# Optimization experiments

Hardware: AMD Instinct MI355X
Metric: run time of the kernel (lower is better)

Reference implementation:

```python
import jax, jax.numpy as jnp
import numpy as np

S = 10        # spiking_segment_count
TEMP = 50.0

def setup_inputs() -> dict:
    key = jax.random.key(0)
    ks = jax.random.split(key, 6)
    bs, din, dout = 2048, 1024, 1024
    x = jax.random.normal(ks[0], (bs, din), dtype=jnp.float32)
    t = jax.random.uniform(ks[1], (bs,), dtype=jnp.float32)  # in [0,1) subset of [-1,1]
    scale = 1.0 / np.sqrt(din)
    param_W = jax.random.normal(ks[2], (din, dout * S * 3), dtype=jnp.float32) * scale
    param_b = jax.random.normal(ks[3], (dout * S * 3,), dtype=jnp.float32) * 0.01
    norm_W = jax.random.normal(ks[4], (din, dout), dtype=jnp.float32) * scale
    norm_b = jax.random.normal(ks[5], (dout,), dtype=jnp.float32) * 0.01
    return {"x": x, "t": t, "param_W": param_W, "param_b": param_b,
            "norm_W": norm_W, "norm_b": norm_b}

def reference(x, t, param_W, param_b, norm_W, norm_b):
    bs = x.shape[0]
    dout = norm_W.shape[1]
    # param GEMM -> (bs, S, dout, 3)
    params = (x @ param_W + param_b).reshape(bs, S, dout, 3)
    weights = jax.nn.softmax(params[..., 0], axis=1)                 # (bs, S, dout)
    keypoints = jnp.concatenate(
        [jnp.zeros_like(weights[:, :1]), jnp.cumsum(weights, axis=1)], axis=1
    ) * 2.0 - 1.0                                                    # (bs, S+1, dout)
    slopes = jnp.tanh(params[..., 1])
    intercepts = params[..., 2]
    tt = t.reshape(-1, 1, 1)                                         # (bs, 1, 1)
    starts = keypoints[:, :S]
    ends = keypoints[:, 1:]
    residual = slopes * tt + intercepts                              # (bs, S, dout)
    validity = ((tt >= starts) & (tt < ends)) | ((tt == 1.0) & (ends == 1.0))
    vf = validity.astype(x.dtype)
    left_margin = jnp.sum((tt - starts) * vf, axis=1)                # (bs, dout)
    right_margin = jnp.sum((ends - tt) * vf, axis=1)
    lw = jax.nn.sigmoid(-TEMP * left_margin)
    rw = jax.nn.sigmoid(-TEMP * right_margin)
    lv = jnp.concatenate([vf[:, :1], vf[:, :-1]], axis=1)
    rv = jnp.concatenate([vf[:, 1:], vf[:, -1:]], axis=1)
    sw = -(lw + rw - 1.0)
    result = (lw * jnp.sum(residual * lv, axis=1)
              + sw * jnp.sum(residual * vf, axis=1)
              + rw * jnp.sum(residual * rv, axis=1))
    # norm == 'constant': subtract segment-wise integral, add norm_net(x)
    integral = jnp.sum(0.5 * slopes * (ends * ends - starts * starts)
                       + intercepts * weights, axis=1) * 0.5
    norm_target = x @ norm_W + norm_b
    return result - integral + norm_target
```

## Files before the change

### kernel.cpp

```cpp
#include <hip/hip_runtime.h>
#include <cstdint>
#include <cstddef>

#define BS    2048
#define DIN   1024
#define DOUT  1024
#define SSEG  10
#define NPAR  30720
#define NPK   20480
#define NCOL2 21504
#define NLG   10240
#define TAU   5e-5f
#define WL_CAP 1048576u

typedef _Float16 half_t;
typedef __attribute__((ext_vector_type(8))) _Float16 half8;
typedef __attribute__((ext_vector_type(4))) _Float16 half4;
typedef __attribute__((ext_vector_type(4))) float   floatx4;

__device__ __forceinline__ void gload16(const void* g, void* l) {
  __builtin_amdgcn_global_load_lds(
      (const __attribute__((address_space(1))) void*)g,
      (__attribute__((address_space(3))) void*)l, 16, 0, 0);
}

__global__ void k_zero(unsigned* c) { if (threadIdx.x == 0) *c = 0; }

__global__ __launch_bounds__(256) void k_split_x(const float* __restrict__ x,
                                                 half_t* __restrict__ xh,
                                                 half_t* __restrict__ xl) {
  int i = blockIdx.x * 256 + threadIdx.x;
  floatx4 v = ((const floatx4*)x)[i];
  half4 h, l;
  #pragma unroll
  for (int c = 0; c < 4; c++) { h[c] = (half_t)v[c]; l[c] = (half_t)(v[c] - (float)h[c]); }
  ((half4*)xh)[i] = h;
  ((half4*)xl)[i] = l;
}

__global__ __launch_bounds__(256) void k_transpose_pk(const float* __restrict__ src,
                                                      half_t* __restrict__ dst) {
  __shared__ float tile[32][33];
  int tx = threadIdx.x & 31;
  int ty = threadIdx.x >> 5;
  int c0 = blockIdx.x * 32;
  int k0 = blockIdx.y * 32;
  int j = c0 + tx;
  int s = j >> 11, rem = j & 2047;
  int scol = s * 3072 + 3 * (rem >> 1) + 1 + (rem & 1);
  #pragma unroll
  for (int r = ty; r < 32; r += 8)
    tile[r][tx] = src[(size_t)(k0 + r) * NPAR + scol];
  __syncthreads();
  #pragma unroll
  for (int r = ty; r < 32; r += 8)
    dst[(size_t)(c0 + r) * DIN + k0 + tx] = (half_t)tile[tx][r];
}

__global__ __launch_bounds__(256) void k_transpose(const float* __restrict__ src,
                                                   half_t* __restrict__ dst,
                                                   int ncols, int col_off) {
  __shared__ float tile[32][33];
  int tx = threadIdx.x & 31;
  int ty = threadIdx.x >> 5;
  int col0 = blockIdx.x * 32;
  int k0   = blockIdx.y * 32;
  #pragma unroll
  for (int r = ty; r < 32; r += 8)
    tile[r][tx] = src[(size_t)(k0 + r) * ncols + col0 + tx];
  __syncthreads();
  #pragma unroll
  for (int r = ty; r < 32; r += 8)
    dst[(size_t)(col0 + r + col_off) * DIN + k0 + tx] = (half_t)tile[tx][r];
}

__global__ __launch_bounds__(256) void k_transpose_logit(const float* __restrict__ src,
                                                         half_t* __restrict__ dh,
                                                         half_t* __restrict__ dl,
                                                         float* __restrict__ wlt) {
  __shared__ float tile[32][33];
  int tx = threadIdx.x & 31;
  int ty = threadIdx.x >> 5;
  int c0 = blockIdx.x * 32;
  int k0 = blockIdx.y * 32;
  int lcol = c0 + tx;
  int scol = (lcol >> 10) * 3072 + (lcol & 1023) * 3;
  #pragma unroll
  for (int r = ty; r < 32; r += 8)
    tile[r][tx] = src[(size_t)(k0 + r) * NPAR + scol];
  __syncthreads();
  #pragma unroll
  for (int r = ty; r < 32; r += 8) {
    float raw = tile[tx][r];
    float v = raw * 32.0f;
    half_t h = (half_t)v;
    half_t l = (half_t)(v - (float)h);
    dh [(size_t)(c0 + r) * DIN + k0 + tx] = h;
    dl [(size_t)(c0 + r) * DIN + k0 + tx] = l;
    wlt[(size_t)(c0 + r) * DIN + k0 + tx] = raw;
  }
}

__global__ __launch_bounds__(256) void k_gemm(const half_t* __restrict__ A,
                                              const half_t* __restrict__ B,
                                              float* __restrict__ C,
                                              const float* __restrict__ pb,
                                              const float* __restrict__ nb) {
  __shared__ __attribute__((aligned(16))) half_t As[128 * 32];
  __shared__ __attribute__((aligned(16))) half_t Bs[128 * 32];
  const int K = DIN;
  int m0 = blockIdx.y * 128, n0 = blockIdx.x * 128;
  int tid = threadIdx.x, w = tid >> 6, L = tid & 63;
  int wm = (w >> 1) * 64, wn = (w & 1) * 64;
  int l15 = L & 15, quad = L >> 4;

  const half_t* ga = A + (size_t)(m0 + w * 16 + (L >> 2)) * K + (L & 3) * 8;
  const half_t* gb = B + (size_t)(n0 + w * 16 + (L >> 2)) * K + (L & 3) * 8;
  char* lA = (char*)As + w * 1024;
  char* lB = (char*)Bs + w * 1024;

  floatx4 acc[4][4] = {};

  for (int k0 = 0; k0 < K; k0 += 32) {
    __syncthreads();
    gload16(ga + k0,          lA);
    gload16(ga + 64 * K + k0, lA + 4096);
    gload16(gb + k0,          lB);
    gload16(gb + 64 * K + k0, lB + 4096);
    __syncthreads();

    half8 af[4], bf[4];
    #pragma unroll
    for (int mi = 0; mi < 4; mi++)
      af[mi] = *(const half8*)((const char*)As + (wm + mi * 16 + l15) * 64 + quad * 16);
    #pragma unroll
    for (int ni = 0; ni < 4; ni++)
      bf[ni] = *(const half8*)((const char*)Bs + (wn + ni * 16 + l15) * 64 + quad * 16);
    #pragma unroll
    for (int mi = 0; mi < 4; mi++)
      #pragma unroll
      for (int ni = 0; ni < 4; ni++)
        acc[mi][ni] = __builtin_amdgcn_mfma_f32_16x16x32_f16(af[mi], bf[ni], acc[mi][ni], 0, 0, 0);
  }

  #pragma unroll
  for (int ni = 0; ni < 4; ni++) {
    int col = n0 + wn + ni * 16 + l15;
    float bias;
    if (col < NPK) {
      int s = col >> 11, rem = col & 2047;
      bias = pb[s * 3072 + 3 * (rem >> 1) + 1 + (rem & 1)];
    } else {
      bias = nb[col - NPK];
    }
    #pragma unroll
    for (int mi = 0; mi < 4; mi++) {
      int row = m0 + wm + mi * 16 + quad * 4;
      floatx4 v = acc[mi][ni];
      #pragma unroll
      for (int r = 0; r < 4; r++)
        C[(size_t)(row + r) * NCOL2 + col] = v[r] + bias;
    }
  }
}

__global__ __launch_bounds__(256) void k_gemm_logit(const half_t* __restrict__ Ah,
                                                    const half_t* __restrict__ Al,
                                                    const half_t* __restrict__ Bh,
                                                    const half_t* __restrict__ Bl,
                                                    float* __restrict__ Lg,
                                                    const float* __restrict__ pb) {
  __shared__ __attribute__((aligned(16))) half_t sAh[128 * 32];
  __shared__ __attribute__((aligned(16))) half_t sAl[128 * 32];
  __shared__ __attribute__((aligned(16))) half_t sBh[128 * 32];
  __shared__ __attribute__((aligned(16))) half_t sBl[128 * 32];
  const int K = DIN;
  int m0 = blockIdx.y * 128, n0 = blockIdx.x * 128;
  int tid = threadIdx.x, w = tid >> 6, L = tid & 63;
  int wm = (w >> 1) * 64, wn = (w & 1) * 64;
  int l15 = L & 15, quad = L >> 4;

  size_t aoff = (size_t)(m0 + w * 16 + (L >> 2)) * K + (L & 3) * 8;
  size_t boff = (size_t)(n0 + w * 16 + (L >> 2)) * K + (L & 3) * 8;
  char* lah = (char*)sAh + w * 1024;
  char* lal = (char*)sAl + w * 1024;
  char* lbh = (char*)sBh + w * 1024;
  char* lbl = (char*)sBl + w * 1024;

  floatx4 acc[4][4] = {};

  for (int k0 = 0; k0 < K; k0 += 32) {
    __syncthreads();
    gload16(Ah + aoff + k0,          lah);
    gload16(Ah + aoff + 64 * K + k0, lah + 4096);
    gload16(Al + aoff + k0,          lal);
    gload16(Al + aoff + 64 * K + k0, lal + 4096);
    gload16(Bh + boff + k0,          lbh);
    gload16(Bh + boff + 64 * K + k0, lbh + 4096);
    gload16(Bl + boff + k0,          lbl);
    gload16(Bl + boff + 64 * K + k0, lbl + 4096);
    __syncthreads();

    #pragma unroll
    for (int mi = 0; mi < 4; mi++) {
      half8 afh = *(const half8*)((const char*)sAh + (wm + mi * 16 + l15) * 64 + quad * 16);
      half8 afl = *(const half8*)((const char*)sAl + (wm + mi * 16 + l15) * 64 + quad * 16);
      #pragma unroll
      for (int ni = 0; ni < 4; ni++) {
        half8 bfh = *(const half8*)((const char*)sBh + (wn + ni * 16 + l15) * 64 + quad * 16);
        half8 bfl = *(const half8*)((const char*)sBl + (wn + ni * 16 + l15) * 64 + quad * 16);
        floatx4 a = acc[mi][ni];
        a = __builtin_amdgcn_mfma_f32_16x16x32_f16(afh, bfh, a, 0, 0, 0);
        a = __builtin_amdgcn_mfma_f32_16x16x32_f16(afl, bfh, a, 0, 0, 0);
        a = __builtin_amdgcn_mfma_f32_16x16x32_f16(afh, bfl, a, 0, 0, 0);
        acc[mi][ni] = a;
      }
    }
  }

  #pragma unroll
  for (int ni = 0; ni < 4; ni++) {
    int col = n0 + wn + ni * 16 + l15;
    float bias = pb[(col >> 10) * 3072 + (col & 1023) * 3];
    #pragma unroll
    for (int mi = 0; mi < 4; mi++) {
      int row = m0 + wm + mi * 16 + quad * 4;
      floatx4 v = acc[mi][ni];
      #pragma unroll
      for (int r = 0; r < 4; r++)
        Lg[(size_t)(row + r) * NLG + col] = v[r] * 0.03125f + bias;
    }
  }
}

__device__ __forceinline__ float spiking_eval(const float* p, float tt, float* mind) {
  float mx = -1e30f;
  #pragma unroll
  for (int s = 0; s < SSEG; s++) mx = fmaxf(mx, p[3 * s]);
  float ew[10], wsum = 0.0f;
  #pragma unroll
  for (int s = 0; s < SSEG; s++) { ew[s] = __expf(p[3 * s] - mx); wsum += ew[s]; }
  float inv = 1.0f / wsum;

  float kp[11];
  kp[0] = -1.0f;
  float cum = 0.0f, md = 1e30f;
  #pragma unroll
  for (int s = 0; s < SSEG; s++) {
    cum += ew[s] * inv;
    kp[s + 1] = cum * 2.0f - 1.0f;
    md = fminf(md, fabsf(tt - kp[s + 1]));
  }
  *mind = md;

  float vf[10], resid[10];
  float lm = 0.0f, rm = 0.0f, integ = 0.0f;
  #pragma unroll
  for (int s = 0; s < SSEG; s++) {
    float p1 = p[3 * s + 1], p2 = p[3 * s + 2];
    float e2 = __expf(2.0f * fabsf(p1));
    float th = copysignf(1.0f - 2.0f / (e2 + 1.0f), p1);
    resid[s] = th * tt + p2;
    float st = kp[s], en = kp[s + 1];
    bool v = ((tt >= st) && (tt < en)) || ((tt == 1.0f) && (en == 1.0f));
    float vv = v ? 1.0f : 0.0f;
    vf[s] = vv;
    lm += (tt - st) * vv;
    rm += (en - tt) * vv;
    integ += 0.5f * th * (en * en - st * st) + p2 * (ew[s] * inv);
  }
  float resLV = 0.0f, resV = 0.0f, resRV = 0.0f;
  #pragma unroll
  for (int s = 0; s < SSEG; s++) {
    float lv = (s == 0) ? vf[0] : vf[s - 1];
    float rv = (s == 9) ? vf[9] : vf[s + 1];
    resLV += resid[s] * lv;
    resV  += resid[s] * vf[s];
    resRV += resid[s] * rv;
  }
  float lw = 1.0f / (1.0f + __expf(50.0f * lm));
  float rw = 1.0f / (1.0f + __expf(50.0f * rm));
  float swt = 1.0f - lw - rw;
  return lw * resLV + swt * resV + rw * resRV - 0.5f * integ + p[30];
}

__global__ __launch_bounds__(256) void k_pointwise(const float* __restrict__ P,
                                                   const float* __restrict__ Lg,
                                                   const float* __restrict__ t,
                                                   float* __restrict__ out,
                                                   unsigned* __restrict__ cnt,
                                                   unsigned* __restrict__ wl,
                                                   unsigned cap) {
  __shared__ __attribute__((aligned(16))) float sp[SSEG * 512];
  int b = blockIdx.x, dg = blockIdx.y, tid = threadIdx.x;
  const float* Pb = P + (size_t)b * NCOL2;
  for (int i = tid; i < SSEG * 128; i += 256) {
    int s = i >> 7, e = i & 127;
    ((floatx4*)sp)[s * 128 + e] = ((const floatx4*)(Pb + s * 2048 + dg * 512))[e];
  }
  float tt = t[b];
  float nt = Pb[NPK + dg * 256 + tid];
  const float* Lb = Lg + (size_t)b * NLG + dg * 256 + tid;
  __syncthreads();

  float p[31];
  #pragma unroll
  for (int s = 0; s < SSEG; s++) {
    p[3 * s]     = Lb[s * 1024];
    p[3 * s + 1] = sp[s * 512 + 2 * tid];
    p[3 * s + 2] = sp[s * 512 + 2 * tid + 1];
  }
  p[30] = nt;
  float mind;
  float r = spiking_eval(p, tt, &mind);
  int d = dg * 256 + tid;
  out[(size_t)b * DOUT + d] = r;
  if (wl != nullptr && mind < TAU) {
    unsigned idx = atomicAdd(cnt, 1u);
    if (idx < cap) wl[idx] = ((unsigned)b << 10) | (unsigned)d;
  }
}

__global__ __launch_bounds__(256) void k_naive(const float* __restrict__ x,
                                               const float* __restrict__ t,
                                               const float* __restrict__ pW,
                                               const float* __restrict__ pb,
                                               const float* __restrict__ nW,
                                               const float* __restrict__ nb,
                                               float* __restrict__ out,
                                               unsigned* __restrict__ cnt,
                                               unsigned* __restrict__ wl,
                                               unsigned cap) {
  __shared__ float xs[DIN];
  int b = blockIdx.x, dg = blockIdx.y, tid = threadIdx.x;
  for (int i = tid; i < DIN; i += 256) xs[i] = x[(size_t)b * DIN + i];
  __syncthreads();
  int d = dg * 256 + tid;
  float acc[31];
  #pragma unroll
  for (int i = 0; i < 31; i++) acc[i] = 0.0f;
  for (int k = 0; k < DIN; k++) {
    float xv = xs[k];
    const float* wr = pW + (size_t)k * NPAR + 3 * d;
    #pragma unroll
    for (int s = 0; s < SSEG; s++) {
      acc[3 * s]     += xv * wr[s * 3072];
      acc[3 * s + 1] += xv * wr[s * 3072 + 1];
      acc[3 * s + 2] += xv * wr[s * 3072 + 2];
    }
    acc[30] += xv * nW[(size_t)k * DOUT + d];
  }
  #pragma unroll
  for (int s = 0; s < SSEG; s++) {
    acc[3 * s]     += pb[s * 3072 + 3 * d];
    acc[3 * s + 1] += pb[s * 3072 + 3 * d + 1];
    acc[3 * s + 2] += pb[s * 3072 + 3 * d + 2];
  }
  acc[30] += nb[d];
  float mind;
  float r = spiking_eval(acc, t[b], &mind);
  out[(size_t)b * DOUT + d] = r;
  if (wl != nullptr && mind < TAU) {
    unsigned idx = atomicAdd(cnt, 1u);
    if (idx < cap) wl[idx] = ((unsigned)b << 10) | (unsigned)d;
  }
}

__global__ __launch_bounds__(256) void k_redo(const float* __restrict__ x,
                                              const float* __restrict__ t,
                                              const float* __restrict__ pW,
                                              const float* __restrict__ pb,
                                              const float* __restrict__ nW,
                                              const float* __restrict__ nb,
                                              const float* __restrict__ P,
                                              const float* __restrict__ WLt,
                                              int haveP,
                                              const unsigned* __restrict__ cnt,
                                              const unsigned* __restrict__ wl,
                                              unsigned cap,
                                              float* __restrict__ out) {
  unsigned n = *cnt;
  if (n > cap) n = cap;
  int lane = threadIdx.x & 63;
  unsigned wave = (blockIdx.x * 256 + threadIdx.x) >> 6;
  unsigned nwaves = (gridDim.x * 256) >> 6;

  for (unsigned e = wave; e < n; e += nwaves) {
    unsigned code = wl[e];
    int b = (int)(code >> 10), d = (int)(code & 1023);

    double lg[10], sl[10], ic[10], nt = 0.0;
    #pragma unroll
    for (int s = 0; s < SSEG; s++) { lg[s] = 0.0; sl[s] = 0.0; ic[s] = 0.0; }

    if (haveP) {
      for (int k = lane; k < DIN; k += 64) {
        double xv = (double)x[(size_t)b * DIN + k];
        #pragma unroll
        for (int s = 0; s < SSEG; s++)
          lg[s] += xv * (double)WLt[(size_t)(s * 1024 + d) * DIN + k];
      }
    } else {
      for (int k = lane; k < DIN; k += 64) {
        double xv = (double)x[(size_t)b * DIN + k];
        const float* wr = pW + (size_t)k * NPAR + 3 * d;
        #pragma unroll
        for (int s = 0; s < SSEG; s++) {
          lg[s] += xv * (double)wr[s * 3072];
          sl[s] += xv * (double)wr[s * 3072 + 1];
          ic[s] += xv * (double)wr[s * 3072 + 2];
        }
        nt += xv * (double)nW[(size_t)k * DOUT + d];
      }
    }
    #pragma unroll
    for (int off = 32; off > 0; off >>= 1) {
      #pragma unroll
      for (int s = 0; s < SSEG; s++) lg[s] += __shfl_down(lg[s], off);
      if (!haveP) {
        #pragma unroll
        for (int s = 0; s < SSEG; s++) {
          sl[s] += __shfl_down(sl[s], off);
          ic[s] += __shfl_down(ic[s], off);
        }
        nt += __shfl_down(nt, off);
      }
    }

    if (lane == 0) {
      double slope[10], icpt[10], ntv;
      if (haveP) {
        const float* Pr = P + (size_t)b * NCOL2;
        #pragma unroll
        for (int s = 0; s < SSEG; s++) {
          slope[s] = tanh((double)Pr[s * 2048 + 2 * d]);
          icpt[s]  = (double)Pr[s * 2048 + 2 * d + 1];
        }
        ntv = (double)Pr[NPK + d];
      } else {
        #pragma unroll
        for (int s = 0; s < SSEG; s++) {
          slope[s] = tanh(sl[s] + (double)pb[s * 3072 + 3 * d + 1]);
          icpt[s]  = ic[s] + (double)pb[s * 3072 + 3 * d + 2];
        }
        ntv = nt + (double)nb[d];
      }
      #pragma unroll
      for (int s = 0; s < SSEG; s++) lg[s] += (double)pb[s * 3072 + 3 * d];

      double mx = -1e300;
      #pragma unroll
      for (int s = 0; s < SSEG; s++) mx = fmax(mx, lg[s]);
      double ew[10], ws = 0.0;
      #pragma unroll
      for (int s = 0; s < SSEG; s++) { ew[s] = exp(lg[s] - mx); ws += ew[s]; }

      double kp[11];
      kp[0] = -1.0;
      double cum = 0.0;
      #pragma unroll
      for (int s = 0; s < SSEG; s++) { cum += ew[s] / ws; kp[s + 1] = cum * 2.0 - 1.0; }

      double tt = (double)t[b];
      double vf[10], resid[10], lm = 0.0, rm = 0.0, integ = 0.0;
      #pragma unroll
      for (int s = 0; s < SSEG; s++) {
        double st = kp[s], en = kp[s + 1];
        bool v = ((tt >= st) && (tt < en)) || ((tt == 1.0) && (en == 1.0));
        double vv = v ? 1.0 : 0.0;
        vf[s] = vv;
        resid[s] = slope[s] * tt + icpt[s];
        lm += (tt - st) * vv;
        rm += (en - tt) * vv;
        integ += 0.5 * slope[s] * (en * en - st * st) + icpt[s] * (ew[s] / ws);
      }
      double rLV = 0.0, rV = 0.0, rRV = 0.0;
      #pragma unroll
      for (int s = 0; s < SSEG; s++) {
        double lv = (s == 0) ? vf[0] : vf[s - 1];
        double rv = (s == 9) ? vf[9] : vf[s + 1];
        rLV += resid[s] * lv;
        rV  += resid[s] * vf[s];
        rRV += resid[s] * rv;
      }
      double lw = 1.0 / (1.0 + exp(50.0 * lm));
      double rw = 1.0 / (1.0 + exp(50.0 * rm));
      double res = lw * rLV + (1.0 - lw - rw) * rV + rw * rRV - 0.5 * integ + ntv;
      out[(size_t)b * DOUT + d] = (float)res;
    }
  }
}

extern "C" void kernel_launch(void* const* d_in, const int* in_sizes, int n_in,
                              void* d_out, int out_size, void* d_ws, size_t ws_size,
                              hipStream_t stream) {
  const float* x  = (const float*)d_in[0];
  const float* t  = (const float*)d_in[1];
  const float* pW = (const float*)d_in[2];
  const float* pb = (const float*)d_in[3];
  const float* nW = (const float*)d_in[4];
  const float* nb = (const float*)d_in[5];
  float* out = (float*)d_out;

  const size_t o_cnt = 0;
  const size_t o_wl  = 64;
  const size_t o_xh  = o_wl  + (size_t)WL_CAP * 4;
  const size_t o_xl  = o_xh  + (size_t)BS * DIN * 2;
  const size_t o_wt  = o_xl  + (size_t)BS * DIN * 2;
  const size_t o_wh  = o_wt  + (size_t)NCOL2 * DIN * 2;
  const size_t o_wlo = o_wh  + (size_t)NLG * DIN * 2;
  const size_t o_wlt = o_wlo + (size_t)NLG * DIN * 2;
  const size_t o_p   = o_wlt + (size_t)NLG * DIN * 4;
  const size_t o_lg  = o_p   + (size_t)BS * NCOL2 * 4;
  const size_t need  = o_lg  + (size_t)BS * NLG * 4;

  bool have_wl = ws_size >= 1024 * 1024;
  unsigned* cnt = (unsigned*)((char*)d_ws + o_cnt);
  unsigned* wl  = (unsigned*)((char*)d_ws + o_wl);
  unsigned cap  = 0;
  if (have_wl) {
    size_t avail = (ws_size >= need) ? (size_t)WL_CAP
                                     : (ws_size - o_wl) / 4;
    cap = (unsigned)(avail < WL_CAP ? avail : WL_CAP);
    k_zero<<<1, 64, 0, stream>>>(cnt);
  }

  if (ws_size >= need) {
    half_t* xh  = (half_t*)((char*)d_ws + o_xh);
    half_t* xl  = (half_t*)((char*)d_ws + o_xl);
    half_t* wt  = (half_t*)((char*)d_ws + o_wt);
    half_t* wh  = (half_t*)((char*)d_ws + o_wh);
    half_t* wlo = (half_t*)((char*)d_ws + o_wlo);
    float*  wlt = (float*)((char*)d_ws + o_wlt);
    float*  P   = (float*)((char*)d_ws + o_p);
    float*  Lg  = (float*)((char*)d_ws + o_lg);

    k_split_x<<<(BS * DIN) / 1024, 256, 0, stream>>>(x, xh, xl);
    k_transpose_pk<<<dim3(NPK / 32, DIN / 32), 256, 0, stream>>>(pW, wt);
    k_transpose<<<dim3(DOUT / 32, DIN / 32), 256, 0, stream>>>(nW, wt, DOUT, NPK);
    k_transpose_logit<<<dim3(NLG / 32, DIN / 32), 256, 0, stream>>>(pW, wh, wlo, wlt);
    k_gemm<<<dim3(NCOL2 / 128, BS / 128), 256, 0, stream>>>(xh, wt, P, pb, nb);
    k_gemm_logit<<<dim3(NLG / 128, BS / 128), 256, 0, stream>>>(xh, xl, wh, wlo, Lg, pb);
    k_pointwise<<<dim3(BS, DOUT / 256), 256, 0, stream>>>(P, Lg, t, out, cnt,
                                                          have_wl ? wl : nullptr, cap);
    if (have_wl)
      k_redo<<<256, 256, 0, stream>>>(x, t, pW, pb, nW, nb, P, wlt, 1, cnt, wl, cap, out);
  } else {
    k_naive<<<dim3(BS, DOUT / 256), 256, 0, stream>>>(x, t, pW, pb, nW, nb, out, cnt,
                                                      have_wl ? wl : nullptr, cap);
    if (have_wl)
      k_redo<<<256, 256, 0, stream>>>(x, t, pW, pb, nW, nb, nullptr, nullptr, 0,
                                      cnt, wl, cap, out);
  }
}
```

Measured before the change: 642.4 us.

## Fuse weight transposes and both GEMMs into single launches, store P as fp16

The two param-weight transpose kernels are merged into one kernel that reads each 384-column chunk of param_W once with vectorised loads and writes the logit hi/lo, raw and slope/intercept layouts. The two GEMM kernels become one launch whose blocks pick between the 3-MFMA split-precision logit path and the plain fp16 path by block index, so the two GEMMs can run concurrently. The slope/intercept/norm GEMM output P is now stored as fp16 to halve its write and read traffic in the pointwise and redo kernels. The counter reset moves into k_split_x to drop a launch. Rounding P to fp16 may change accuracy near segment boundaries, which the redo path only partly covers.

```diff
diff --git a/kernel.cpp b/kernel.cpp
--- a/kernel.cpp
+++ b/kernel.cpp
@@ -10,12 +10,15 @@
 #define NPK   20480
 #define NCOL2 21504
 #define NLG   10240
+#define NT_LG 80
+#define NT_SM 168
 #define TAU   5e-5f
 #define WL_CAP 1048576u
 
 typedef _Float16 half_t;
 typedef __attribute__((ext_vector_type(8))) _Float16 half8;
 typedef __attribute__((ext_vector_type(4))) _Float16 half4;
+typedef __attribute__((ext_vector_type(2))) _Float16 half2v;
 typedef __attribute__((ext_vector_type(4))) float   floatx4;
 
 __device__ __forceinline__ void gload16(const void* g, void* l) {
@@ -28,7 +31,9 @@
 
 __global__ __launch_bounds__(256) void k_split_x(const float* __restrict__ x,
                                                  half_t* __restrict__ xh,
-                                                 half_t* __restrict__ xl) {
+                                                 half_t* __restrict__ xl,
+                                                 unsigned* __restrict__ cnt) {
+  if (blockIdx.x == 0 && threadIdx.x == 0) *cnt = 0;
   int i = blockIdx.x * 256 + threadIdx.x;
   floatx4 v = ((const floatx4*)x)[i];
   half4 h, l;
@@ -38,23 +43,44 @@
   ((half4*)xl)[i] = l;
 }
 
-__global__ __launch_bounds__(256) void k_transpose_pk(const float* __restrict__ src,
-                                                      half_t* __restrict__ dst) {
-  __shared__ float tile[32][33];
-  int tx = threadIdx.x & 31;
-  int ty = threadIdx.x >> 5;
-  int c0 = blockIdx.x * 32;
+__global__ __launch_bounds__(256) void k_transw(const float* __restrict__ src,
+                                                half_t* __restrict__ wsm,
+                                                half_t* __restrict__ wh,
+                                                half_t* __restrict__ wlo,
+                                                float* __restrict__ wlt) {
+  __shared__ float tile[32][384];
+  int bx = blockIdx.x;
   int k0 = blockIdx.y * 32;
-  int j = c0 + tx;
-  int s = j >> 11, rem = j & 2047;
-  int scol = s * 3072 + 3 * (rem >> 1) + 1 + (rem & 1);
-  #pragma unroll
-  for (int r = ty; r < 32; r += 8)
-    tile[r][tx] = src[(size_t)(k0 + r) * NPAR + scol];
+  int tid = threadIdx.x;
+  int s  = bx >> 3;
+  int d0 = (bx & 7) * 128;
+  const float* sb = src + (size_t)k0 * NPAR + bx * 384;
+  for (int i = tid; i < 32 * 96; i += 256) {
+    int r = i / 96, q = i - r * 96;
+    ((floatx4*)&tile[r][0])[q] = ((const floatx4*)(sb + (size_t)r * NPAR))[q];
+  }
   __syncthreads();
-  #pragma unroll
-  for (int r = ty; r < 32; r += 8)
-    dst[(size_t)(c0 + r) * DIN + k0 + tx] = (half_t)tile[tx][r];
+  int j   = tid & 127;
+  int ks  = (tid >> 7) * 16;
+  {
+    size_t row = (size_t)(s * 1024 + d0 + j) * DIN + k0 + ks;
+    #pragma unroll
+    for (int m = 0; m < 16; m++) {
+      float raw = tile[ks + m][3 * j];
+      float v = raw * 32.0f;
+      half_t h = (half_t)v;
+      wlt[row + m] = raw;
+      wh [row + m] = h;
+      wlo[row + m] = (half_t)(v - (float)h);
+    }
+  }
+  #pragma unroll
+  for (int c = 0; c < 2; c++) {
+    size_t row = (size_t)(s * 2048 + 2 * (d0 + j) + c) * DIN + k0 + ks;
+    #pragma unroll
+    for (int m = 0; m < 16; m++)
+      wsm[row + m] = (half_t)tile[ks + m][3 * j + 1 + c];
+  }
 }
 
 __global__ __launch_bounds__(256) void k_transpose(const float* __restrict__ src,
@@ -74,161 +100,124 @@
     dst[(size_t)(col0 + r + col_off) * DIN + k0 + tx] = (half_t)tile[tx][r];
 }
 
-__global__ __launch_bounds__(256) void k_transpose_logit(const float* __restrict__ src,
-                                                         half_t* __restrict__ dh,
-                                                         half_t* __restrict__ dl,
-                                                         float* __restrict__ wlt) {
-  __shared__ float tile[32][33];
-  int tx = threadIdx.x & 31;
-  int ty = threadIdx.x >> 5;
-  int c0 = blockIdx.x * 32;
-  int k0 = blockIdx.y * 32;
-  int lcol = c0 + tx;
-  int scol = (lcol >> 10) * 3072 + (lcol & 1023) * 3;
-  #pragma unroll
-  for (int r = ty; r < 32; r += 8)
-    tile[r][tx] = src[(size_t)(k0 + r) * NPAR + scol];
-  __syncthreads();
-  #pragma unroll
-  for (int r = ty; r < 32; r += 8) {
-    float raw = tile[tx][r];
-    float v = raw * 32.0f;
-    half_t h = (half_t)v;
-    half_t l = (half_t)(v - (float)h);
-    dh [(size_t)(c0 + r) * DIN + k0 + tx] = h;
-    dl [(size_t)(c0 + r) * DIN + k0 + tx] = l;
-    wlt[(size_t)(c0 + r) * DIN + k0 + tx] = raw;
-  }
-}
-
-__global__ __launch_bounds__(256) void k_gemm(const half_t* __restrict__ A,
-                                              const half_t* __restrict__ B,
-                                              float* __restrict__ C,
-                                              const float* __restrict__ pb,
-                                              const float* __restrict__ nb) {
-  __shared__ __attribute__((aligned(16))) half_t As[128 * 32];
-  __shared__ __attribute__((aligned(16))) half_t Bs[128 * 32];
+__global__ __launch_bounds__(256) void k_gemm_all(const half_t* __restrict__ Ah,
+                                                  const half_t* __restrict__ Al,
+                                                  const half_t* __restrict__ Wsm,
+                                                  const half_t* __restrict__ Bh,
+                                                  const half_t* __restrict__ Bl,
+                                                  half_t* __restrict__ P,
+                                                  float* __restrict__ Lg,
+                                                  const float* __restrict__ pb,
+                                                  const float* __restrict__ nb) {
+  __shared__ __attribute__((aligned(16))) half_t s0[128 * 32];
+  __shared__ __attribute__((aligned(16))) half_t s1[128 * 32];
+  __shared__ __attribute__((aligned(16))) half_t s2[128 * 32];
+  __shared__ __attribute__((aligned(16))) half_t s3[128 * 32];
   const int K = DIN;
-  int m0 = blockIdx.y * 128, n0 = blockIdx.x * 128;
+  int bx = blockIdx.x;
+  int m0 = blockIdx.y * 128;
   int tid = threadIdx.x, w = tid >> 6, L = tid & 63;
   int wm = (w >> 1) * 64, wn = (w & 1) * 64;
   int l15 = L & 15, quad = L >> 4;
 
-  const half_t* ga = A + (size_t)(m0 + w * 16 + (L >> 2)) * K + (L & 3) * 8;
-  const half_t* gb = B + (size_t)(n0 + w * 16 + (L >> 2)) * K + (L & 3) * 8;
-  char* lA = (char*)As + w * 1024;
-  char* lB = (char*)Bs + w * 1024;
+  size_t arow = (size_t)(m0 + w * 16 + (L >> 2)) * K + (L & 3) * 8;
+  char* l0 = (char*)s0 + w * 1024;
+  char* l1 = (char*)s1 + w * 1024;
+  char* l2 = (char*)s2 + w * 1024;
+  char* l3 = (char*)s3 + w * 1024;
 
   floatx4 acc[4][4] = {};
 
-  for (int k0 = 0; k0 < K; k0 += 32) {
-    __syncthreads();
-    gload16(ga + k0,          lA);
-    gload16(ga + 64 * K + k0, lA + 4096);
-    gload16(gb + k0,          lB);
-    gload16(gb + 64 * K + k0, lB + 4096);
-    __syncthreads();
-
-    half8 af[4], bf[4];
-    #pragma unroll
-    for (int mi = 0; mi < 4; mi++)
-      af[mi] = *(const half8*)((const char*)As + (wm + mi * 16 + l15) * 64 + quad * 16);
-    #pragma unroll
-    for (int ni = 0; ni < 4; ni++)
-      bf[ni] = *(const half8*)((const char*)Bs + (wn + ni * 16 + l15) * 64 + quad * 16);
-    #pragma unroll
-    for (int mi = 0; mi < 4; mi++)
+  if (bx < NT_LG) {
+    int n0 = bx * 128;
+    size_t brow = (size_t)(n0 + w * 16 + (L >> 2)) * K + (L & 3) * 8;
+
+    for (int k0 = 0; k0 < K; k0 += 32) {
+      __syncthreads();
+      gload16(Ah + arow + k0,          l0);
+      gload16(Ah + arow + 64 * K + k0, l0 + 4096);
+      gload16(Al + arow + k0,          l1);
+      gload16(Al + arow + 64 * K + k0, l1 + 4096);
+      gload16(Bh + brow + k0,          l2);
+      gload16(Bh + brow + 64 * K + k0, l2 + 4096);
+      gload16(Bl + brow + k0,          l3);
+      gload16(Bl + brow + 64 * K + k0, l3 + 4096);
+      __syncthreads();
+
+      #pragma unroll
+      for (int mi = 0; mi < 4; mi++) {
+        half8 afh = *(const half8*)((const char*)s0 + (wm + mi * 16 + l15) * 64 + quad * 16);
+        half8 afl = *(const half8*)((const char*)s1 + (wm + mi * 16 + l15) * 64 + quad * 16);
+        #pragma unroll
+        for (int ni = 0; ni < 4; ni++) {
+          half8 bfh = *(const half8*)((const char*)s2 + (wn + ni * 16 + l15) * 64 + quad * 16);
+          half8 bfl = *(const half8*)((const char*)s3 + (wn + ni * 16 + l15) * 64 + quad * 16);
+          floatx4 a = acc[mi][ni];
+          a = __builtin_amdgcn_mfma_f32_16x16x32_f16(afh, bfh, a, 0, 0, 0);
+          a = __builtin_amdgcn_mfma_f32_16x16x32_f16(afl, bfh, a, 0, 0, 0);
+          a = __builtin_amdgcn_mfma_f32_16x16x32_f16(afh, bfl, a, 0, 0, 0);
+          acc[mi][ni] = a;
+        }
+      }
+    }
+
+    #pragma unroll
+    for (int ni = 0; ni < 4; ni++) {
+      int col = n0 + wn + ni * 16 + l15;
+      float bias = pb[(col >> 10) * 3072 + (col & 1023) * 3];
+      #pragma unroll
+      for (int mi = 0; mi < 4; mi++) {
+        int row = m0 + wm + mi * 16 + quad * 4;
+        floatx4 v = acc[mi][ni];
+        #pragma unroll
+        for (int r = 0; r < 4; r++)
+          Lg[(size_t)(row + r) * NLG + col] = v[r] * 0.03125f + bias;
+      }
+    }
+  } else {
+    int n0 = (bx - NT_LG) * 128;
+    size_t brow = (size_t)(n0 + w * 16 + (L >> 2)) * K + (L & 3) * 8;
+
+    for (int k0 = 0; k0 < K; k0 += 32) {
+      __syncthreads();
+      gload16(Ah + arow + k0,           l0);
+      gload16(Ah + arow + 64 * K + k0,  l0 + 4096);
+      gload16(Wsm + brow + k0,          l2);
+      gload16(Wsm + brow + 64 * K + k0, l2 + 4096);
+      __syncthreads();
+
+      half8 af[4], bf[4];
+      #pragma unroll
+      for (int mi = 0; mi < 4; mi++)
+        af[mi] = *(const half8*)((const char*)s0 + (wm + mi * 16 + l15) * 64 + quad * 16);
       #pragma unroll
       for (int ni = 0; ni < 4; ni++)
-        acc[mi][ni] = __builtin_amdgcn_mfma_f32_16x16x32_f16(af[mi], bf[ni], acc[mi][ni], 0, 0, 0);
-  }
-
-  #pragma unroll
-  for (int ni = 0; ni < 4; ni++) {
-    int col = n0 + wn + ni * 16 + l15;
-    float bias;
-    if (col < NPK) {
-      int s = col >> 11, rem = col & 2047;
-      bias = pb[s * 3072 + 3 * (rem >> 1) + 1 + (rem & 1)];
-    } else {
-      bias = nb[col - NPK];
-    }
-    #pragma unroll
-    for (int mi = 0; mi < 4; mi++) {
-      int row = m0 + wm + mi * 16 + quad * 4;
-      floatx4 v = acc[mi][ni];
-      #pragma unroll
-      for (int r = 0; r < 4; r++)
-        C[(size_t)(row + r) * NCOL2 + col] = v[r] + bias;
-    }
-  }
-}
-
-__global__ __launch_bounds__(256) void k_gemm_logit(const half_t* __restrict__ Ah,
-                                                    const half_t* __restrict__ Al,
-                                                    const half_t* __restrict__ Bh,
-                                                    const half_t* __restrict__ Bl,
-                                                    float* __restrict__ Lg,
-                                                    const float* __restrict__ pb) {
-  __shared__ __attribute__((aligned(16))) half_t sAh[128 * 32];
-  __shared__ __attribute__((aligned(16))) half_t sAl[128 * 32];
-  __shared__ __attribute__((aligned(16))) half_t sBh[128 * 32];
-  __shared__ __attribute__((aligned(16))) half_t sBl[128 * 32];
-  const int K = DIN;
-  int m0 = blockIdx.y * 128, n0 = blockIdx.x * 128;
-  int tid = threadIdx.x, w = tid >> 6, L = tid & 63;
-  int wm = (w >> 1) * 64, wn = (w & 1) * 64;
-  int l15 = L & 15, quad = L >> 4;
-
-  size_t aoff = (size_t)(m0 + w * 16 + (L >> 2)) * K + (L & 3) * 8;
-  size_t boff = (size_t)(n0 + w * 16 + (L >> 2)) * K + (L & 3) * 8;
-  char* lah = (char*)sAh + w * 1024;
-  char* lal = (char*)sAl + w * 1024;
-  char* lbh = (char*)sBh + w * 1024;
-  char* lbl = (char*)sBl + w * 1024;
-
-  floatx4 acc[4][4] = {};
-
-  for (int k0 = 0; k0 < K; k0 += 32) {
-    __syncthreads();
-    gload16(Ah + aoff + k0,          lah);
-    gload16(Ah + aoff + 64 * K + k0, lah + 4096);
-    gload16(Al + aoff + k0,          lal);
-    gload16(Al + aoff + 64 * K + k0, lal + 4096);
-    gload16(Bh + boff + k0,          lbh);
-    gload16(Bh + boff + 64 * K + k0, lbh + 4096);
-    gload16(Bl + boff + k0,          lbl);
-    gload16(Bl + boff + 64 * K + k0, lbl + 4096);
-    __syncthreads();
-
-    #pragma unroll
-    for (int mi = 0; mi < 4; mi++) {
-      half8 afh = *(const half8*)((const char*)sAh + (wm + mi * 16 + l15) * 64 + quad * 16);
-      half8 afl = *(const half8*)((const char*)sAl + (wm + mi * 16 + l15) * 64 + quad * 16);
-      #pragma unroll
-      for (int ni = 0; ni < 4; ni++) {
-        half8 bfh = *(const half8*)((const char*)sBh + (wn + ni * 16 + l15) * 64 + quad * 16);
-        half8 bfl = *(const half8*)((const char*)sBl + (wn + ni * 16 + l15) * 64 + quad * 16);
-        floatx4 a = acc[mi][ni];
-        a = __builtin_amdgcn_mfma_f32_16x16x32_f16(afh, bfh, a, 0, 0, 0);
-        a = __builtin_amdgcn_mfma_f32_16x16x32_f16(afl, bfh, a, 0, 0, 0);
-        a = __builtin_amdgcn_mfma_f32_16x16x32_f16(afh, bfl, a, 0, 0, 0);
-        acc[mi][ni] = a;
-      }
-    }
-  }
-
-  #pragma unroll
-  for (int ni = 0; ni < 4; ni++) {
-    int col = n0 + wn + ni * 16 + l15;
-    float bias = pb[(col >> 10) * 3072 + (col & 1023) * 3];
-    #pragma unroll
-    for (int mi = 0; mi < 4; mi++) {
-      int row = m0 + wm + mi * 16 + quad * 4;
-      floatx4 v = acc[mi][ni];
-      #pragma unroll
-      for (int r = 0; r < 4; r++)
-        Lg[(size_t)(row + r) * NLG + col] = v[r] * 0.03125f + bias;
+        bf[ni] = *(const half8*)((const char*)s2 + (wn + ni * 16 + l15) * 64 + quad * 16);
+      #pragma unroll
+      for (int mi = 0; mi < 4; mi++)
+        #pragma unroll
+        for (int ni = 0; ni < 4; ni++)
+          acc[mi][ni] = __builtin_amdgcn_mfma_f32_16x16x32_f16(af[mi], bf[ni], acc[mi][ni], 0, 0, 0);
+    }
+
+    #pragma unroll
+    for (int ni = 0; ni < 4; ni++) {
+      int col = n0 + wn + ni * 16 + l15;
+      float bias;
+      if (col < NPK) {
+        int s = col >> 11, rem = col & 2047;
+        bias = pb[s * 3072 + 3 * (rem >> 1) + 1 + (rem & 1)];
+      } else {
+        bias = nb[col - NPK];
+      }
+      #pragma unroll
+      for (int mi = 0; mi < 4; mi++) {
+        int row = m0 + wm + mi * 16 + quad * 4;
+        floatx4 v = acc[mi][ni];
+        #pragma unroll
+        for (int r = 0; r < 4; r++)
+          P[(size_t)(row + r) * NCOL2 + col] = (half_t)(v[r] + bias);
+      }
     }
   }
 }
@@ -284,31 +273,32 @@
   return lw * resLV + swt * resV + rw * resRV - 0.5f * integ + p[30];
 }
 
-__global__ __launch_bounds__(256) void k_pointwise(const float* __restrict__ P,
+__global__ __launch_bounds__(256) void k_pointwise(const half_t* __restrict__ P,
                                                    const float* __restrict__ Lg,
                                                    const float* __restrict__ t,
                                                    float* __restrict__ out,
                                                    unsigned* __restrict__ cnt,
                                                    unsigned* __restrict__ wl,
                                                    unsigned cap) {
-  __shared__ __attribute__((aligned(16))) float sp[SSEG * 512];
+  __shared__ __attribute__((aligned(16))) half_t sp[SSEG * 512];
   int b = blockIdx.x, dg = blockIdx.y, tid = threadIdx.x;
-  const float* Pb = P + (size_t)b * NCOL2;
-  for (int i = tid; i < SSEG * 128; i += 256) {
-    int s = i >> 7, e = i & 127;
-    ((floatx4*)sp)[s * 128 + e] = ((const floatx4*)(Pb + s * 2048 + dg * 512))[e];
+  const half_t* Pb = P + (size_t)b * NCOL2;
+  for (int i = tid; i < SSEG * 64; i += 256) {
+    int s = i >> 6, e = i & 63;
+    ((uint4*)sp)[(s << 6) + e] = ((const uint4*)(Pb + s * 2048 + dg * 512))[e];
   }
   float tt = t[b];
-  float nt = Pb[NPK + dg * 256 + tid];
+  float nt = (float)Pb[NPK + dg * 256 + tid];
   const float* Lb = Lg + (size_t)b * NLG + dg * 256 + tid;
   __syncthreads();
 
   float p[31];
   #pragma unroll
   for (int s = 0; s < SSEG; s++) {
-    p[3 * s]     = Lb[s * 1024];
-    p[3 * s + 1] = sp[s * 512 + 2 * tid];
-    p[3 * s + 2] = sp[s * 512 + 2 * tid + 1];
+    p[3 * s] = Lb[s * 1024];
+    half2v hv = ((const half2v*)sp)[s * 256 + tid];
+    p[3 * s + 1] = (float)hv.x;
+    p[3 * s + 2] = (float)hv.y;
   }
   p[30] = nt;
   float mind;
@@ -372,7 +362,7 @@
                                               const float* __restrict__ pb,
                                               const float* __restrict__ nW,
                                               const float* __restrict__ nb,
-                                              const float* __restrict__ P,
+                                              const half_t* __restrict__ P,
                                               const float* __restrict__ WLt,
                                               int haveP,
                                               const unsigned* __restrict__ cnt,
@@ -430,13 +420,13 @@
     if (lane == 0) {
       double slope[10], icpt[10], ntv;
       if (haveP) {
-        const float* Pr = P + (size_t)b * NCOL2;
+        const half_t* Pr = P + (size_t)b * NCOL2;
         #pragma unroll
         for (int s = 0; s < SSEG; s++) {
-          slope[s] = tanh((double)Pr[s * 2048 + 2 * d]);
-          icpt[s]  = (double)Pr[s * 2048 + 2 * d + 1];
+          slope[s] = tanh((double)(float)Pr[s * 2048 + 2 * d]);
+          icpt[s]  = (double)(float)Pr[s * 2048 + 2 * d + 1];
         }
-        ntv = (double)Pr[NPK + d];
+        ntv = (double)(float)Pr[NPK + d];
       } else {
         #pragma unroll
         for (int s = 0; s < SSEG; s++) {
@@ -506,12 +496,12 @@
   const size_t o_wl  = 64;
   const size_t o_xh  = o_wl  + (size_t)WL_CAP * 4;
   const size_t o_xl  = o_xh  + (size_t)BS * DIN * 2;
-  const size_t o_wt  = o_xl  + (size_t)BS * DIN * 2;
-  const size_t o_wh  = o_wt  + (size_t)NCOL2 * DIN * 2;
+  const size_t o_wsm = o_xl  + (size_t)BS * DIN * 2;
+  const size_t o_wh  = o_wsm + (size_t)NCOL2 * DIN * 2;
   const size_t o_wlo = o_wh  + (size_t)NLG * DIN * 2;
   const size_t o_wlt = o_wlo + (size_t)NLG * DIN * 2;
   const size_t o_p   = o_wlt + (size_t)NLG * DIN * 4;
-  const size_t o_lg  = o_p   + (size_t)BS * NCOL2 * 4;
+  const size_t o_lg  = o_p   + (size_t)BS * NCOL2 * 2;
   const size_t need  = o_lg  + (size_t)BS * NLG * 4;
 
   bool have_wl = ws_size >= 1024 * 1024;
@@ -522,30 +512,29 @@
     size_t avail = (ws_size >= need) ? (size_t)WL_CAP
                                      : (ws_size - o_wl) / 4;
     cap = (unsigned)(avail < WL_CAP ? avail : WL_CAP);
-    k_zero<<<1, 64, 0, stream>>>(cnt);
   }
 
   if (ws_size >= need) {
     half_t* xh  = (half_t*)((char*)d_ws + o_xh);
     half_t* xl  = (half_t*)((char*)d_ws + o_xl);
-    half_t* wt  = (half_t*)((char*)d_ws + o_wt);
+    half_t* wsm = (half_t*)((char*)d_ws + o_wsm);
     half_t* wh  = (half_t*)((char*)d_ws + o_wh);
     half_t* wlo = (half_t*)((char*)d_ws + o_wlo);
     float*  wlt = (float*)((char*)d_ws + o_wlt);
-    float*  P   = (float*)((char*)d_ws + o_p);
+    half_t* P   = (half_t*)((char*)d_ws + o_p);
     float*  Lg  = (float*)((char*)d_ws + o_lg);
 
-    k_split_x<<<(BS * DIN) / 1024, 256, 0, stream>>>(x, xh, xl);
-    k_transpose_pk<<<dim3(NPK / 32, DIN / 32), 256, 0, stream>>>(pW, wt);
-    k_transpose<<<dim3(DOUT / 32, DIN / 32), 256, 0, stream>>>(nW, wt, DOUT, NPK);
-    k_transpose_logit<<<dim3(NLG / 32, DIN / 32), 256, 0, stream>>>(pW, wh, wlo, wlt);
-    k_gemm<<<dim3(NCOL2 / 128, BS / 128), 256, 0, stream>>>(xh, wt, P, pb, nb);
-    k_gemm_logit<<<dim3(NLG / 128, BS / 128), 256, 0, stream>>>(xh, xl, wh, wlo, Lg, pb);
+    k_split_x<<<(BS * DIN) / 1024, 256, 0, stream>>>(x, xh, xl, cnt);
+    k_transw<<<dim3(NPAR / 384, DIN / 32), 256, 0, stream>>>(pW, wsm, wh, wlo, wlt);
+    k_transpose<<<dim3(DOUT / 32, DIN / 32), 256, 0, stream>>>(nW, wsm, DOUT, NPK);
+    k_gemm_all<<<dim3(NT_LG + NT_SM, BS / 128), 256, 0, stream>>>(xh, xl, wsm, wh, wlo,
+                                                                  P, Lg, pb, nb);
     k_pointwise<<<dim3(BS, DOUT / 256), 256, 0, stream>>>(P, Lg, t, out, cnt,
                                                           have_wl ? wl : nullptr, cap);
     if (have_wl)
       k_redo<<<256, 256, 0, stream>>>(x, t, pW, pb, nW, nb, P, wlt, 1, cnt, wl, cap, out);
   } else {
+    if (have_wl) k_zero<<<1, 64, 0, stream>>>(cnt);
     k_naive<<<dim3(BS, DOUT / 256), 256, 0, stream>>>(x, t, pW, pb, nW, nb, out, cnt,
                                                       have_wl ? wl : nullptr, cap);
     if (have_wl)
```

Result: no change. 629.9 us (-1.9%).
